# Kernel optimization log

Measured on AMD Instinct MI355X. Metric: run time of the kernel, lower is better.

Reference implementation:

```python
import jax, jax.numpy as jnp
import numpy as np

B, FIN, V, X, Y, Z = 2, 32, 768, 8, 8, 8
K, FOUT = 5, 32
NNZ = V * 8  # ~8 neighbors per vertex


def setup_inputs() -> dict:
    key = jax.random.key(0)
    k1, k2, k3, k4, k5 = jax.random.split(key, 5)
    std = np.sqrt(2.0 / (FIN * K)).astype(np.float32)
    return {
        "lap_rows": jax.random.randint(k1, (NNZ,), 0, V, dtype=jnp.int32),
        "lap_cols": jax.random.randint(k2, (NNZ,), 0, V, dtype=jnp.int32),
        "lap_vals": jax.random.normal(k3, (NNZ,), dtype=jnp.float32) * 0.1,
        "x": jax.random.normal(k4, (B, FIN, V, X, Y, Z), dtype=jnp.float32),
        "weight": jax.random.normal(k5, (K, FIN, FOUT), dtype=jnp.float32) * std,
        "bias": jnp.full((FOUT,), 0.01, dtype=jnp.float32),
    }


def reference(lap_rows, lap_cols, lap_vals, x, weight, bias):
    Bb, Fin, Vv, Xx, Yy, Zz = x.shape
    Kk, _, Fout = weight.shape

    def spmm(v):  # sparse [V,V] @ dense [V,D]
        return jax.ops.segment_sum(lap_vals[:, None] * v[lap_cols],
                                   lap_rows, num_segments=Vv)

    # [B,Fin,V,X,Y,Z] -> [V, Fin*B*X*Y*Z]
    x0 = jnp.transpose(x, (2, 1, 0, 3, 4, 5)).reshape(Vv, -1)
    xs = [x0]
    if Kk > 1:
        x1 = spmm(x0)
        xs.append(x1)
        for _ in range(2, Kk):
            x2 = 2.0 * spmm(x1) - x0
            xs.append(x2)
            x0, x1 = x1, x2
    basis = jnp.stack(xs, axis=0)  # [K, V, Fin*B*X*Y*Z]
    basis = basis.reshape(Kk, Vv, Fin, Bb, Xx, Yy, Zz)
    basis = jnp.transpose(basis, (3, 1, 4, 5, 6, 0, 2))  # [B,V,X,Y,Z,K,Fin]
    out = basis.reshape(-1, Kk * Fin) @ weight.reshape(Kk * Fin, Fout)
    out = out.reshape(Bb, Vv, Xx, Yy, Zz, Fout)
    out = jnp.transpose(out, (0, 5, 1, 2, 3, 4))  # [B,Fout,V,X,Y,Z]
    return out + bias[None, :, None, None, None, None]
```

## Files before the change

kernel.cpp:

```cpp
#include <hip/hip_runtime.h>
#include <stdint.h>

#define V      768
#define FINC   32
#define FOUTC  32
#define XYZ    512
#define NB     2
#define ROWP   40
#define MAXDEG 32
#define EROWS  36

typedef unsigned short u16;
typedef unsigned int   u32;
typedef short bf16x8 __attribute__((ext_vector_type(8)));
typedef float f32x4  __attribute__((ext_vector_type(4)));
typedef float f32x2  __attribute__((ext_vector_type(2)));

__device__ __forceinline__ u16 f2bf(float f) {
  u32 u = __float_as_uint(f);
  u32 r = u + 0x7fffu + ((u >> 16) & 1u);
  return (u16)(r >> 16);
}
__device__ __forceinline__ float bflo(u32 w) { return __uint_as_float(w << 16); }
__device__ __forceinline__ float bfhi(u32 w) { return __uint_as_float(w & 0xffff0000u); }
__device__ __forceinline__ float bfhi_raw(u32 w) { return __uint_as_float(w); }
__device__ __forceinline__ u32 cvtpk_bf16(float lo, float hi) {
  u32 r;
  asm("v_cvt_pk_bf16_f32 %0, %1, %2" : "=v"(r) : "v"(lo), "v"(hi));
  return r;
}

__global__ __launch_bounds__(64) void build_ell(const int* __restrict__ rows,
                                                const int* __restrict__ cols,
                                                const float* __restrict__ vals,
                                                int nnz,
                                                int2* __restrict__ epair,
                                                int* __restrict__ deg) {
  int v = blockIdx.x;
  int lane = threadIdx.x;
  int cnt = 0;
  for (int base = 0; base < nnz; base += 64) {
    int i = base + lane;
    bool m = (i < nnz) && (rows[i] == v);
    unsigned long long mask = __ballot(m);
    if (m) {
      int pos = cnt + __popcll(mask & ((1ull << lane) - 1ull));
      if (pos < MAXDEG)
        epair[v * MAXDEG + pos] = make_int2(cols[i], __float_as_int(vals[i]));
    }
    cnt += __popcll(mask);
  }
  int d = cnt < MAXDEG ? cnt : MAXDEG;
  for (int p = d + lane; p < MAXDEG; p += 64)
    epair[v * MAXDEG + p] = make_int2(0, 0);
  if (lane == 0) deg[v] = d;
}

__global__ __launch_bounds__(V) void sort_rows(const int* __restrict__ deg,
                                               int* __restrict__ perm,
                                               int* __restrict__ inv_g,
                                               int* __restrict__ wtrip) {
  __shared__ int sdeg[V];
  int v = threadIdx.x;
  int d = deg[v];
  sdeg[v] = d;
  __syncthreads();
  int r = 0;
  for (int u = 0; u < V; ++u) {
    int du = sdeg[u];
    r += (du > d) || (du == d && u < v);
  }
  const unsigned long long GPK = 0x8495A6B73210ull;
  int w = (int)((GPK >> (4 * (r >> 6))) & 15ull);
  int p = w * 64 + (r & 63);
  perm[p] = v;
  inv_g[v] = p;
  if ((r & 63) == 0) wtrip[w] = d;
}

#define TXV 12
__global__ __launch_bounds__(512) void transpose_x(const float* __restrict__ x,
                                                   const int* __restrict__ perm,
                                                   const int* __restrict__ deg,
                                                   const int2* __restrict__ epair,
                                                   const int* __restrict__ inv_g,
                                                   int2* __restrict__ ep3,
                                                   u16* __restrict__ xT) {
  __shared__ u32 TL2[384 * 34];
  __shared__ int PV[TXV];
  int g = blockIdx.x;
  int t = threadIdx.x;
  if (g < EROWS) {
    int e = g;
    for (int p = t; p < V; p += 512) {
      int v = perm[p];
      int d = deg[v];
      int2 o = make_int2(0, 0);
      if (e < d) {
        int2 pe = epair[v * MAXDEG + e];
        o = make_int2(inv_g[pe.x] * (ROWP * 2), pe.y);
      }
      ep3[e * V + p] = o;
    }
  }
  int b = g >> 9, pvt = (g >> 3) & 63, xt = g & 7;
  int pv0 = pvt * TXV;
  int xyz0 = xt * 64;
  if (t < TXV) PV[t] = perm[pv0 + t];
  __syncthreads();
  int q = t & 15;
  int rgrp = t >> 4;
#pragma unroll
  for (int st = 0; st < 12; ++st) {
    int row = st * 32 + rgrp;
    int vloc = row >> 5, f = row & 31;
    const float4 xv = *(const float4*)&x[((size_t)(b * FINC + f) * V + PV[vloc]) * XYZ + xyz0 + 4 * q];
    u32 A = cvtpk_bf16(xv.x, xv.y);
    u32 B = cvtpk_bf16(xv.z, xv.w);
    *(uint2*)&TL2[row * 34 + 2 * q] = make_uint2(A, B);
  }
  __syncthreads();
  const u16* TL16 = (const u16*)TL2;
  int s = t & 7, xyz = t >> 3;
  u32* dst = (u32*)(xT + ((size_t)(b * XYZ + xyz0 + xyz) * V + pv0) * FINC);
#pragma unroll
  for (int it = 0; it < 24; ++it) {
    int i = s + 8 * it;
    u32 lo = TL16[(2 * i) * 68 + xyz];
    u32 hi = TL16[(2 * i + 1) * 68 + xyz];
    dst[i] = lo | (hi << 16);
  }
}

__global__ __launch_bounds__(1024, 4) void cheb_main(
    const u16* __restrict__ xT, const int2* __restrict__ ep3,
    const int* __restrict__ perm, const int* __restrict__ wtrip,
    const float* __restrict__ weight, const float* __restrict__ bias,
    u32* __restrict__ stage) {
  __shared__ __align__(16) u16   CUR[V * ROWP];
  __shared__ __align__(16) u16   PRV[V * ROWP];
  __shared__ __align__(16) uint4 WF[5][2][64];
  __shared__ u16 PRM[V];
  __shared__ int WT[12];

  int g = blockIdx.x;
  int xcd = g & 7;
  int u = g >> 3;
  int phase = u >> 5;
  int xyz = xcd * 32 + (u & 31) + (phase & 1) * 256;
  int b = phase >> 1;
  int slice = b * XYZ + xyz;

  int tid = threadIdx.x;
  int lane = tid & 63;
  int w = tid >> 6;
  int l15 = lane & 15, l4 = lane >> 4;
  bool gath = tid < V;

  if (tid < 640) {
    int k = tid >> 7, n = (tid >> 6) & 1, ln = tid & 63;
    int a15 = ln & 15, a4 = ln >> 4;
    u32 pw[4];
#pragma unroll
    for (int p = 0; p < 4; ++p) {
      float w0 = weight[(size_t)(k * FINC + a4 * 8 + 2 * p) * FOUTC + n * 16 + a15];
      float w1 = weight[(size_t)(k * FINC + a4 * 8 + 2 * p + 1) * FOUTC + n * 16 + a15];
      pw[p] = (u32)f2bf(w0) | ((u32)f2bf(w1) << 16);
    }
    WF[k][n][ln] = make_uint4(pw[0], pw[1], pw[2], pw[3]);
  }
  if (tid < 12) WT[tid] = wtrip[tid];
  if (gath) PRM[tid] = (u16)perm[tid];
  float bsv[2] = {bias[l15], bias[16 + l15]};

  if (gath) {
    const uint4* src = (const uint4*)(xT + (size_t)slice * V * FINC) + tid * 4;
    uint4* dst = (uint4*)(CUR + tid * ROWP);
#pragma unroll
    for (int j = 0; j < 4; ++j) dst[j] = src[j];
  }
  __syncthreads();

  int trip = 0;
  if (w < 12) trip = __builtin_amdgcn_readfirstlane(WT[w]);
  const int2* pp = ep3 + tid;

  f32x4 acc[3][2];
#pragma unroll
  for (int a = 0; a < 3; ++a)
#pragma unroll
    for (int n = 0; n < 2; ++n) acc[a][n] = (f32x4){0.f, 0.f, 0.f, 0.f};

  auto gemm_acc = [&](int k) {
    bf16x8 bn0 = *(const bf16x8*)&WF[k][0][lane];
    bf16x8 bn1 = *(const bf16x8*)&WF[k][1][lane];
#pragma unroll
    for (int a = 0; a < 3; ++a) {
      int row = w * 48 + a * 16 + l15;
      bf16x8 af = *(const bf16x8*)(CUR + row * ROWP + l4 * 8);
      acc[a][0] = __builtin_amdgcn_mfma_f32_16x16x32_bf16(af, bn0, acc[a][0], 0, 0, 0);
      acc[a][1] = __builtin_amdgcn_mfma_f32_16x16x32_bf16(af, bn1, acc[a][1], 0, 0, 0);
    }
  };

  f32x2 fa2[16];
  auto fma_edge = [&](float fv, uint4 qa, uint4 qb, uint4 qc, uint4 qd) {
    f32x2 fv2 = {fv, fv};
    u32 wq[16] = {qa.x, qa.y, qa.z, qa.w, qb.x, qb.y, qb.z, qb.w,
                  qc.x, qc.y, qc.z, qc.w, qd.x, qd.y, qd.z, qd.w};
#pragma unroll
    for (int p = 0; p < 16; ++p) {
      f32x2 s = {bflo(wq[p]), bfhi_raw(wq[p])};
      fa2[p] += fv2 * s;
    }
  };
  auto gather = [&]() {
#pragma unroll
    for (int j = 0; j < 16; ++j) fa2[j] = (f32x2){0.f, 0.f};
    int trips = (trip + 1) & ~1;
    int2 r0 = pp[0], r1 = pp[V], r2 = pp[2 * V];
    const uint4* s0 = (const uint4*)((const char*)CUR + (u32)r0.x);
    uint4 A0 = s0[0], A1 = s0[1], A2 = s0[2], A3 = s0[3];
    for (int e = 0; e < trips; e += 2) {
      const uint4* s1 = (const uint4*)((const char*)CUR + (u32)r1.x);
      uint4 B0 = s1[0], B1 = s1[1], B2 = s1[2], B3 = s1[3];
      int2 n3 = pp[(e + 3) * V];
      fma_edge(__int_as_float(r0.y), A0, A1, A2, A3);
      const uint4* s2 = (const uint4*)((const char*)CUR + (u32)r2.x);
      A0 = s2[0]; A1 = s2[1]; A2 = s2[2]; A3 = s2[3];
      int2 n4 = pp[(e + 4) * V];
      fma_edge(__int_as_float(r1.y), B0, B1, B2, B3);
      r0 = r2; r1 = n3; r2 = n4;
    }
  };

  auto do_update = [&](bool first) {
    uint4* cp = (uint4*)(CUR + tid * ROWP);
    uint4* qp = (uint4*)(PRV + tid * ROWP);
    uint4 c[4];
#pragma unroll
    for (int j = 0; j < 4; ++j) c[j] = cp[j];
    u32 npk[16];
    if (first) {
#pragma unroll
      for (int j = 0; j < 16; ++j) npk[j] = cvtpk_bf16(fa2[j][0], fa2[j][1]);
    } else {
      uint4 pv[4];
#pragma unroll
      for (int j = 0; j < 4; ++j) pv[j] = qp[j];
      u32 wp[16] = {pv[0].x, pv[0].y, pv[0].z, pv[0].w, pv[1].x, pv[1].y, pv[1].z, pv[1].w,
                    pv[2].x, pv[2].y, pv[2].z, pv[2].w, pv[3].x, pv[3].y, pv[3].z, pv[3].w};
#pragma unroll
      for (int j = 0; j < 16; ++j) {
        float t0 = 2.f * fa2[j][0] - bflo(wp[j]);
        float t1 = 2.f * fa2[j][1] - bfhi(wp[j]);
        npk[j] = cvtpk_bf16(t0, t1);
      }
    }
#pragma unroll
    for (int j = 0; j < 4; ++j) {
      qp[j] = c[j];
      cp[j] = make_uint4(npk[4 * j], npk[4 * j + 1], npk[4 * j + 2], npk[4 * j + 3]);
    }
  };

#pragma unroll
  for (int ph = 0; ph <= 3; ++ph) {
    gemm_acc(ph);
    if (gath) gather();
    __syncthreads();
    if (gath) do_update(ph == 0);
    __syncthreads();
  }

  gemm_acc(4);

  u32* stg = stage + (size_t)slice * (V * 16);
#pragma unroll
  for (int a = 0; a < 3; ++a) {
#pragma unroll
    for (int r = 0; r < 4; ++r) {
      int vr = PRM[w * 48 + a * 16 + l4 * 4 + r];
      u32 pk = cvtpk_bf16(acc[a][0][r] + bsv[0], acc[a][1][r] + bsv[1]);
      stg[vr * 16 + l15] = pk;
    }
  }
}

#define TO_VT  12
#define TO_PAD 193
__global__ __launch_bounds__(512) void transpose_out(const u32* __restrict__ stage,
                                                     float* __restrict__ out) {
  __shared__ u32 T[64 * TO_PAD];
  int g = blockIdx.x;
  int b = g >> 9, vt = (g >> 3) & 63, xt = g & 7;
  int v0 = vt * TO_VT;
  int xyz0 = xt * 64;
  int t = threadIdx.x;
  const u32* base = stage + (size_t)(b * XYZ + xyz0) * (V * 16) + v0 * 16;
#pragma unroll
  for (int i = 0; i < 6; ++i) {
    int idx4 = i * 512 + t;
    int j = idx4 / 48;
    int c4 = idx4 - j * 48;
    uint4 q = *(const uint4*)(base + (size_t)j * (V * 16) + c4 * 4);
    int w0 = c4 * 4;
    T[j * TO_PAD + w0]     = q.x;
    T[j * TO_PAD + w0 + 1] = q.y;
    T[j * TO_PAD + w0 + 2] = q.z;
    T[j * TO_PAD + w0 + 3] = q.w;
  }
  __syncthreads();
  int xyz2 = t & 31;
  int grp = t >> 5;
#pragma unroll
  for (int i = 0; i < 24; ++i) {
    int fout = grp * 2 + (i & 1);
    int vv = i >> 1;
    int col = vv * 16 + (fout & 15);
    u32 pka = T[(2 * xyz2) * TO_PAD + col];
    u32 pkb = T[(2 * xyz2 + 1) * TO_PAD + col];
    float va = (fout < 16) ? bflo(pka) : bfhi(pka);
    float vb = (fout < 16) ? bflo(pkb) : bfhi(pkb);
    *(float2*)&out[((size_t)(b * FOUTC + fout) * V + v0 + vv) * XYZ + xyz0 + 2 * xyz2] =
        make_float2(va, vb);
  }
}

extern "C" void kernel_launch(void* const* d_in, const int* in_sizes, int n_in,
                              void* d_out, int out_size, void* d_ws, size_t ws_size,
                              hipStream_t stream) {
  const int*   lap_rows = (const int*)d_in[0];
  const int*   lap_cols = (const int*)d_in[1];
  const float* lap_vals = (const float*)d_in[2];
  const float* x        = (const float*)d_in[3];
  const float* weight   = (const float*)d_in[4];
  const float* bias     = (const float*)d_in[5];
  float* out = (float*)d_out;
  int nnz = in_sizes[0];

  char* ws = (char*)d_ws;
  const size_t XT_BYTES = (size_t)NB * XYZ * V * FINC * sizeof(u16);
  const size_t EP_BYTES = (size_t)V * MAXDEG * 8;
  const size_t E3_BYTES = (size_t)EROWS * V * 8;
  u16*  xT    = (u16*)ws;
  u32*  stg   = (u32*)ws;
  int2* epair = (int2*)(ws + XT_BYTES);
  int2* ep3   = (int2*)(ws + XT_BYTES + EP_BYTES);
  int*  deg   = (int*)(ws + XT_BYTES + EP_BYTES + E3_BYTES);
  int*  perm  = (int*)(ws + XT_BYTES + EP_BYTES + E3_BYTES + 3072);
  int*  inv_g = (int*)(ws + XT_BYTES + EP_BYTES + E3_BYTES + 6144);
  int*  wtrip = (int*)(ws + XT_BYTES + EP_BYTES + E3_BYTES + 9216);

  hipLaunchKernelGGL(build_ell, dim3(V), dim3(64), 0, stream,
                     lap_rows, lap_cols, lap_vals, nnz, epair, deg);
  hipLaunchKernelGGL(sort_rows, dim3(1), dim3(V), 0, stream,
                     deg, perm, inv_g, wtrip);
  hipLaunchKernelGGL(transpose_x, dim3(NB * 64 * 8), dim3(512), 0, stream,
                     x, perm, deg, epair, inv_g, ep3, xT);
  hipLaunchKernelGGL(cheb_main, dim3(NB * XYZ), dim3(1024), 0, stream,
                     xT, ep3, perm, wtrip, weight, bias, stg);
  hipLaunchKernelGGL(transpose_out, dim3(NB * 64 * 8), dim3(512), 0, stream,
                     stg, out);
}
```

Baseline: 193.6 us.

## Gather neighbor rows from an fp8 shadow copy and keep previous term in registers

Adds an fp8 (e4m3) copy of the current Chebyshev term in shared memory and has the sparse gather read 32 bytes per neighbor instead of 64, decoding with packed fp8-to-f32 conversions. The previous term is now kept in registers instead of a shared PRV buffer, which frees LDS and removes its read and write traffic. The aim is to halve LDS gather bandwidth. The cost is a large loss of precision in the recurrence inputs, which may fail accuracy tolerances, and extra conversion ALU work.

```diff
diff --git a/kernel.cpp b/kernel.cpp
--- a/kernel.cpp
+++ b/kernel.cpp
@@ -7,6 +7,7 @@
 #define XYZ    512
 #define NB     2
 #define ROWP   40
+#define QROW   48
 #define MAXDEG 32
 #define EROWS  36
 
@@ -23,7 +24,6 @@
 }
 __device__ __forceinline__ float bflo(u32 w) { return __uint_as_float(w << 16); }
 __device__ __forceinline__ float bfhi(u32 w) { return __uint_as_float(w & 0xffff0000u); }
-__device__ __forceinline__ float bfhi_raw(u32 w) { return __uint_as_float(w); }
 __device__ __forceinline__ u32 cvtpk_bf16(float lo, float hi) {
   u32 r;
   asm("v_cvt_pk_bf16_f32 %0, %1, %2" : "=v"(r) : "v"(lo), "v"(hi));
@@ -98,7 +98,7 @@
       int2 o = make_int2(0, 0);
       if (e < d) {
         int2 pe = epair[v * MAXDEG + e];
-        o = make_int2(inv_g[pe.x] * (ROWP * 2), pe.y);
+        o = make_int2(inv_g[pe.x] * QROW, pe.y);
       }
       ep3[e * V + p] = o;
     }
@@ -138,7 +138,7 @@
     const float* __restrict__ weight, const float* __restrict__ bias,
     u32* __restrict__ stage) {
   __shared__ __align__(16) u16   CUR[V * ROWP];
-  __shared__ __align__(16) u16   PRV[V * ROWP];
+  __shared__ __align__(16) unsigned char CURQ[V * QROW];
   __shared__ __align__(16) uint4 WF[5][2][64];
   __shared__ u16 PRM[V];
   __shared__ int WT[12];
@@ -176,8 +176,23 @@
   if (gath) {
     const uint4* src = (const uint4*)(xT + (size_t)slice * V * FINC) + tid * 4;
     uint4* dst = (uint4*)(CUR + tid * ROWP);
-#pragma unroll
-    for (int j = 0; j < 4; ++j) dst[j] = src[j];
+    u32 cw[16], q8[8];
+#pragma unroll
+    for (int j = 0; j < 4; ++j) {
+      uint4 q = src[j];
+      dst[j] = q;
+      cw[4 * j] = q.x; cw[4 * j + 1] = q.y;
+      cw[4 * j + 2] = q.z; cw[4 * j + 3] = q.w;
+    }
+#pragma unroll
+    for (int d = 0; d < 8; ++d) {
+      u32 p0 = cw[2 * d], p1 = cw[2 * d + 1];
+      u32 q = __builtin_amdgcn_cvt_pk_fp8_f32(bflo(p0), bfhi(p0), 0, false);
+      q8[d] = __builtin_amdgcn_cvt_pk_fp8_f32(bflo(p1), bfhi(p1), q, true);
+    }
+    uint4* qp = (uint4*)(CURQ + tid * QROW);
+    qp[0] = make_uint4(q8[0], q8[1], q8[2], q8[3]);
+    qp[1] = make_uint4(q8[4], q8[5], q8[6], q8[7]);
   }
   __syncthreads();
 
@@ -204,14 +219,15 @@
   };
 
   f32x2 fa2[16];
-  auto fma_edge = [&](float fv, uint4 qa, uint4 qb, uint4 qc, uint4 qd) {
+  auto fma_edge8 = [&](float fv, uint4 qa, uint4 qb) {
     f32x2 fv2 = {fv, fv};
-    u32 wq[16] = {qa.x, qa.y, qa.z, qa.w, qb.x, qb.y, qb.z, qb.w,
-                  qc.x, qc.y, qc.z, qc.w, qd.x, qd.y, qd.z, qd.w};
-#pragma unroll
-    for (int p = 0; p < 16; ++p) {
-      f32x2 s = {bflo(wq[p]), bfhi_raw(wq[p])};
-      fa2[p] += fv2 * s;
+    u32 wq[8] = {qa.x, qa.y, qa.z, qa.w, qb.x, qb.y, qb.z, qb.w};
+#pragma unroll
+    for (int d = 0; d < 8; ++d) {
+      f32x2 s0 = __builtin_amdgcn_cvt_pk_f32_fp8(wq[d], false);
+      f32x2 s1 = __builtin_amdgcn_cvt_pk_f32_fp8(wq[d], true);
+      fa2[2 * d]     += fv2 * s0;
+      fa2[2 * d + 1] += fv2 * s1;
     }
   };
   auto gather = [&]() {
@@ -219,57 +235,63 @@
     for (int j = 0; j < 16; ++j) fa2[j] = (f32x2){0.f, 0.f};
     int trips = (trip + 1) & ~1;
     int2 r0 = pp[0], r1 = pp[V], r2 = pp[2 * V];
-    const uint4* s0 = (const uint4*)((const char*)CUR + (u32)r0.x);
-    uint4 A0 = s0[0], A1 = s0[1], A2 = s0[2], A3 = s0[3];
+    const uint4* s0 = (const uint4*)(CURQ + (u32)r0.x);
+    uint4 A0 = s0[0], A1 = s0[1];
     for (int e = 0; e < trips; e += 2) {
-      const uint4* s1 = (const uint4*)((const char*)CUR + (u32)r1.x);
-      uint4 B0 = s1[0], B1 = s1[1], B2 = s1[2], B3 = s1[3];
+      const uint4* s1 = (const uint4*)(CURQ + (u32)r1.x);
+      uint4 B0 = s1[0], B1 = s1[1];
       int2 n3 = pp[(e + 3) * V];
-      fma_edge(__int_as_float(r0.y), A0, A1, A2, A3);
-      const uint4* s2 = (const uint4*)((const char*)CUR + (u32)r2.x);
-      A0 = s2[0]; A1 = s2[1]; A2 = s2[2]; A3 = s2[3];
+      fma_edge8(__int_as_float(r0.y), A0, A1);
+      const uint4* s2 = (const uint4*)(CURQ + (u32)r2.x);
+      A0 = s2[0]; A1 = s2[1];
       int2 n4 = pp[(e + 4) * V];
-      fma_edge(__int_as_float(r1.y), B0, B1, B2, B3);
+      fma_edge8(__int_as_float(r1.y), B0, B1);
       r0 = r2; r1 = n3; r2 = n4;
     }
   };
 
-  auto do_update = [&](bool first) {
-    uint4* cp = (uint4*)(CUR + tid * ROWP);
-    uint4* qp = (uint4*)(PRV + tid * ROWP);
-    uint4 c[4];
-#pragma unroll
-    for (int j = 0; j < 4; ++j) c[j] = cp[j];
-    u32 npk[16];
-    if (first) {
-#pragma unroll
-      for (int j = 0; j < 16; ++j) npk[j] = cvtpk_bf16(fa2[j][0], fa2[j][1]);
-    } else {
-      uint4 pv[4];
-#pragma unroll
-      for (int j = 0; j < 4; ++j) pv[j] = qp[j];
-      u32 wp[16] = {pv[0].x, pv[0].y, pv[0].z, pv[0].w, pv[1].x, pv[1].y, pv[1].z, pv[1].w,
-                    pv[2].x, pv[2].y, pv[2].z, pv[2].w, pv[3].x, pv[3].y, pv[3].z, pv[3].w};
-#pragma unroll
-      for (int j = 0; j < 16; ++j) {
-        float t0 = 2.f * fa2[j][0] - bflo(wp[j]);
-        float t1 = 2.f * fa2[j][1] - bfhi(wp[j]);
-        npk[j] = cvtpk_bf16(t0, t1);
-      }
-    }
-#pragma unroll
-    for (int j = 0; j < 4; ++j) {
-      qp[j] = c[j];
-      cp[j] = make_uint4(npk[4 * j], npk[4 * j + 1], npk[4 * j + 2], npk[4 * j + 3]);
-    }
-  };
+  u32 prevpk[16];
 
 #pragma unroll
   for (int ph = 0; ph <= 3; ++ph) {
     gemm_acc(ph);
     if (gath) gather();
     __syncthreads();
-    if (gath) do_update(ph == 0);
+    if (gath) {
+      uint4* cp = (uint4*)(CUR + tid * ROWP);
+      uint4 c0 = cp[0], c1 = cp[1], c2 = cp[2], c3 = cp[3];
+      u32 cw[16] = {c0.x, c0.y, c0.z, c0.w, c1.x, c1.y, c1.z, c1.w,
+                    c2.x, c2.y, c2.z, c2.w, c3.x, c3.y, c3.z, c3.w};
+      u32 npk[16], q8[8];
+      if (ph == 0) {
+#pragma unroll
+        for (int j = 0; j < 16; ++j) {
+          float t0 = fa2[j][0], t1 = fa2[j][1];
+          npk[j] = cvtpk_bf16(t0, t1);
+          if ((j & 1) == 0) q8[j >> 1] = __builtin_amdgcn_cvt_pk_fp8_f32(t0, t1, 0, false);
+          else              q8[j >> 1] = __builtin_amdgcn_cvt_pk_fp8_f32(t0, t1, q8[j >> 1], true);
+        }
+      } else {
+#pragma unroll
+        for (int j = 0; j < 16; ++j) {
+          u32 pv = prevpk[j];
+          float t0 = 2.f * fa2[j][0] - bflo(pv);
+          float t1 = 2.f * fa2[j][1] - bfhi(pv);
+          npk[j] = cvtpk_bf16(t0, t1);
+          if ((j & 1) == 0) q8[j >> 1] = __builtin_amdgcn_cvt_pk_fp8_f32(t0, t1, 0, false);
+          else              q8[j >> 1] = __builtin_amdgcn_cvt_pk_fp8_f32(t0, t1, q8[j >> 1], true);
+        }
+      }
+#pragma unroll
+      for (int j = 0; j < 16; ++j) prevpk[j] = cw[j];
+      cp[0] = make_uint4(npk[0], npk[1], npk[2], npk[3]);
+      cp[1] = make_uint4(npk[4], npk[5], npk[6], npk[7]);
+      cp[2] = make_uint4(npk[8], npk[9], npk[10], npk[11]);
+      cp[3] = make_uint4(npk[12], npk[13], npk[14], npk[15]);
+      uint4* qp = (uint4*)(CURQ + tid * QROW);
+      qp[0] = make_uint4(q8[0], q8[1], q8[2], q8[3]);
+      qp[1] = make_uint4(q8[4], q8[5], q8[6], q8[7]);
+    }
     __syncthreads();
   }
 
```

Result: faster. 182.2 us (-5.9%).
